# Optimization experiments

Hardware: AMD Instinct MI355X
Metric: run time of the kernel (lower is better)

The kernel has to match this reference:

```python
import jax, jax.numpy as jnp
import numpy as np

N, D, H = 2048, 1024, 16
DH = D // H
LN_EPS = 1e-5


def setup_inputs() -> dict:
    key = jax.random.key(0)
    ks = jax.random.split(key, 12)
    s = 1.0 / np.sqrt(D)
    return {
        "ht": jax.random.normal(ks[0], (N, D), jnp.float32),
        "attention_mask": jnp.ones((1, N), jnp.float32),
        "Wq": jax.random.normal(ks[1], (D, D), jnp.float32) * s,
        "bq": jnp.zeros((D,), jnp.float32),
        "Wk": jax.random.normal(ks[2], (D, D), jnp.float32) * s,
        "bk": jnp.zeros((D,), jnp.float32),
        "Wv": jax.random.normal(ks[3], (D, D), jnp.float32) * s,
        "bv": jnp.zeros((D,), jnp.float32),
        "Wd": jax.random.normal(ks[4], (D, D), jnp.float32) * s,
        "bd": jnp.zeros((D,), jnp.float32),
        "gamma": jnp.ones((D,), jnp.float32),
        "beta": jnp.zeros((D,), jnp.float32),
    }


def reference(ht, attention_mask, Wq, bq, Wk, bk, Wv, bv, Wd, bd, gamma, beta):
    # ht: [N, D] -> batch of 1: [1, N, D]
    x = ht[None]
    # QKV projections, split into heads: [1, N, H, DH]
    q = (x @ Wq.T + bq).reshape(1, N, H, DH)
    k = (x @ Wk.T + bk).reshape(1, N, H, DH)
    v = (x @ Wv.T + bv).reshape(1, N, H, DH)
    # attention scores [1, H, N, N]
    scores = jnp.einsum("bnhd,bmhd->bhnm", q, k) / jnp.sqrt(jnp.asarray(DH, x.dtype))
    # 2D mask -> [B, 1, 1, N], additive form (1 - m) * -10000
    ext_mask = (1.0 - attention_mask)[:, None, None, :] * -10000.0
    scores = scores + ext_mask
    probs = jax.nn.softmax(scores, axis=-1)
    # context [1, N, H, DH] -> [N, D]
    ctx = jnp.einsum("bhnm,bmhd->bnhd", probs, v).reshape(1, N, D)[0]
    # dense + tanh (dropout p=0 is identity) + residual
    sht = jnp.tanh(ctx @ Wd.T + bd) + ht
    # LayerNorm over last dim
    mu = jnp.mean(sht, axis=-1, keepdims=True)
    var = jnp.var(sht, axis=-1, keepdims=True)
    return (sht - mu) / jnp.sqrt(var + LN_EPS) * gamma + beta
```

## Files before the change

kernel.cpp:

```cpp
#include <hip/hip_runtime.h>
#include <hip/hip_bf16.h>
#include <math.h>

#define N_TOK 2048
#define DMODEL 1024
#define NHEAD 16
#define DHEAD 64
#define LN_EPS 1e-5f
#define LOG2E 1.44269504f

typedef __attribute__((ext_vector_type(8))) short short8;
typedef __attribute__((ext_vector_type(4))) short s16x4;
typedef __attribute__((ext_vector_type(4))) float f32x4;
typedef __attribute__((ext_vector_type(16))) float f32x16;

__device__ inline unsigned short f2bf(float f) {
    union { float f; unsigned u; } v; v.f = f;
    unsigned r = v.u + 0x7FFF + ((v.u >> 16) & 1);
    return (unsigned short)(r >> 16);
}

__device__ inline float bf2f(unsigned short b) {
    union { unsigned u; float f; } v; v.u = ((unsigned)b) << 16;
    return v.f;
}

__device__ __forceinline__ unsigned cvtpk_bf16(float lo, float hi) {
    unsigned r;
    asm("v_cvt_pk_bf16_f32 %0, %1, %2" : "=v"(r) : "v"(lo), "v"(hi));
    return r;
}

__device__ __forceinline__ float mx3(float a, float b, float c) {
    return fmaxf(fmaxf(a, b), c);
}

__device__ __forceinline__ void gld16(const unsigned short* g, unsigned short* l) {
    __builtin_amdgcn_global_load_lds(
        (const __attribute__((address_space(1))) unsigned int*)g,
        (__attribute__((address_space(3))) unsigned int*)l, 16, 0, 0);
}

__global__ __launch_bounds__(256) void cvt_all(
    const float* __restrict__ ht, const float* __restrict__ Wq, const float* __restrict__ Wk,
    const float* __restrict__ Wv, const float* __restrict__ Wd, const float* __restrict__ mask,
    unsigned short* __restrict__ Xb, unsigned short* __restrict__ Wqb,
    unsigned short* __restrict__ Wkb, unsigned short* __restrict__ Wvb,
    unsigned short* __restrict__ Wdb, float* __restrict__ madd)
{
    int b = blockIdx.x;
    if (b < 6144) {
        const float* in; unsigned short* out; int off;
        if (b < 2048) { in = ht; out = Xb; off = b * 1024; }
        else {
            int wb = b - 2048; int wi = wb >> 10;
            off = (wb & 1023) * 1024;
            in  = wi == 0 ? Wq  : wi == 1 ? Wk  : wi == 2 ? Wv  : Wd;
            out = wi == 0 ? Wqb : wi == 1 ? Wkb : wi == 2 ? Wvb : Wdb;
        }
        int i = off + threadIdx.x * 4;
        float4 v = *reinterpret_cast<const float4*>(in + i);
        ushort4 o;
        o.x = f2bf(v.x); o.y = f2bf(v.y); o.z = f2bf(v.z); o.w = f2bf(v.w);
        *reinterpret_cast<ushort4*>(out + i) = o;
    } else {
        int i = (b - 6144) * 1024 + threadIdx.x * 4;
        float4 m = *reinterpret_cast<const float4*>(mask + i);
        float4 o;
        o.x = (1.0f - m.x) * (-10000.0f * LOG2E);
        o.y = (1.0f - m.y) * (-10000.0f * LOG2E);
        o.z = (1.0f - m.z) * (-10000.0f * LOG2E);
        o.w = (1.0f - m.w) * (-10000.0f * LOG2E);
        *reinterpret_cast<float4*>(madd + i) = o;
    }
}

__global__ __launch_bounds__(256) void vtrans(const unsigned short* __restrict__ V,
                                              unsigned short* __restrict__ VT) {
    __shared__ unsigned short tile[64][72];
    int n0 = blockIdx.x * 64;
    int d0 = blockIdx.y * 64;
    int t = threadIdx.x;
    int r = t >> 3, c8 = t & 7;
    #pragma unroll
    for (int it = 0; it < 2; ++it) {
        int rr = it * 32 + r;
        short8 v = *reinterpret_cast<const short8*>(V + (size_t)(n0 + rr) * DMODEL + d0 + c8 * 8);
        *reinterpret_cast<short8*>(&tile[rr][c8 * 8]) = v;
    }
    __syncthreads();
    #pragma unroll
    for (int it = 0; it < 2; ++it) {
        int rr = it * 32 + r;
        short8 o;
        #pragma unroll
        for (int j = 0; j < 8; ++j) o[j] = (short)tile[c8 * 8 + j][rr];
        *reinterpret_cast<short8*>(VT + (size_t)(d0 + rr) * N_TOK + n0 + c8 * 8) = o;
    }
}

__global__ __launch_bounds__(256) void gemm_qkv(
    const unsigned short* __restrict__ X,
    const unsigned short* __restrict__ Wq, const unsigned short* __restrict__ Wk,
    const unsigned short* __restrict__ Wv,
    const float* __restrict__ bq, const float* __restrict__ bk, const float* __restrict__ bv,
    unsigned short* __restrict__ Q, unsigned short* __restrict__ K, unsigned short* __restrict__ V)
{
    __shared__ __align__(16) unsigned short As[64 * 64];
    __shared__ __align__(16) unsigned short Bs[128 * 64];
    int row0 = blockIdx.x * 64;
    int col0 = blockIdx.y * 128;
    int mat = col0 >> 10;
    int wcol0 = col0 & 1023;
    const unsigned short* W = mat == 0 ? Wq : (mat == 1 ? Wk : Wv);
    const float* bias = mat == 0 ? bq : (mat == 1 ? bk : bv);
    unsigned short* O = mat == 0 ? Q : (mat == 1 ? K : V);
    float osc = (mat == 0) ? (0.125f * LOG2E) : 1.0f;

    int t = threadIdx.x, w = t >> 6, l = t & 63;
    int lr = l & 15, lk = l >> 4;
    int wc = w * 32;
    int srow = l >> 3, scol = (l & 7) * 8;

    f32x4 acc[4][2] = {};

    for (int k0 = 0; k0 < DMODEL; k0 += 64) {
        #pragma unroll
        for (int c = 0; c < 2; ++c) {
            int ci = (w << 1) | c;
            int r = (ci << 3) | srow;
            gld16(X + (size_t)(row0 + r) * DMODEL + k0 + scol, As + ci * 512);
        }
        #pragma unroll
        for (int c = 0; c < 4; ++c) {
            int ci = (w << 2) | c;
            int r = (ci << 3) | srow;
            gld16(W + (size_t)(wcol0 + r) * DMODEL + k0 + scol, Bs + ci * 512);
        }
        __syncthreads();
        #pragma unroll
        for (int kk = 0; kk < 64; kk += 32) {
            short8 af[4], bf[2];
            #pragma unroll
            for (int m = 0; m < 4; ++m)
                af[m] = *reinterpret_cast<const short8*>(As + (m * 16 + lr) * 64 + kk + (lk << 3));
            #pragma unroll
            for (int n = 0; n < 2; ++n)
                bf[n] = *reinterpret_cast<const short8*>(Bs + (wc + n * 16 + lr) * 64 + kk + (lk << 3));
            #pragma unroll
            for (int m = 0; m < 4; ++m)
                #pragma unroll
                for (int n = 0; n < 2; ++n)
                    acc[m][n] = __builtin_amdgcn_mfma_f32_16x16x32_bf16(af[m], bf[n], acc[m][n], 0, 0, 0);
        }
        __syncthreads();
    }

    #pragma unroll
    for (int n = 0; n < 2; ++n) {
        int ccol = wcol0 + wc + n * 16 + lr;
        float bia = bias[ccol];
        #pragma unroll
        for (int m = 0; m < 4; ++m) {
            #pragma unroll
            for (int r = 0; r < 4; ++r) {
                int rowg = row0 + m * 16 + lk * 4 + r;
                O[(size_t)rowg * DMODEL + ccol] = f2bf((acc[m][n][r] + bia) * osc);
            }
        }
    }
}

__global__ __launch_bounds__(256) void attn32(
    const unsigned short* __restrict__ Q, const unsigned short* __restrict__ K,
    const unsigned short* __restrict__ VT, const float* __restrict__ madd,
    unsigned short* __restrict__ P0, unsigned short* __restrict__ P1,
    float* __restrict__ Mm, float* __restrict__ Ml)
{
    __shared__ __align__(16) unsigned short Kt[2][4096];
    __shared__ __align__(16) unsigned short Vt[2][4096];

    int h = blockIdx.y;
    int hb = h * DHEAD;
    int z = blockIdx.z;
    int kbase = z << 10;
    int t = threadIdx.x, w = t >> 6, l = t & 63;
    int lo5 = l & 31, hi = l >> 5;
    int qw = blockIdx.x * 128 + w * 32;

    short8 qf[4];
    #pragma unroll
    for (int ds = 0; ds < 4; ++ds)
        qf[ds] = *reinterpret_cast<const short8*>(
            Q + (size_t)(qw + lo5) * DMODEL + hb + ds * 16 + hi * 8);

    short8 ones8;
    #pragma unroll
    for (int j = 0; j < 8; ++j) ones8[j] = (short)0x3F80;

    f32x16 ctx0 = {}, ctx1 = {}, ctxS = {};
    float mrow = -1e30f;

#define STAGE(kt_, buf_) do {                                                   \
        int k0s = kbase + (kt_) * 64;                                           \
        _Pragma("unroll")                                                       \
        for (int c = 0; c < 2; ++c) {                                           \
            int ci = (w << 1) | c;                                              \
            int rr = (ci << 3) | (l >> 3);                                      \
            int sc = (((l & 7) ^ (rr & 7)) << 3);                               \
            gld16(K + (size_t)(k0s + rr) * DMODEL + hb + sc, &Kt[buf_][ci * 512]); \
            gld16(VT + (size_t)(hb + rr) * N_TOK + k0s + sc, &Vt[buf_][ci * 512]); \
        }                                                                       \
    } while (0)

    STAGE(0, 0);
    __syncthreads();

    int cb = 0;
    for (int kt = 0; kt < 16; ++kt) {
        f32x16 s0, s1;
        #pragma unroll
        for (int rg = 0; rg < 4; ++rg) {
            f32x4 a = *reinterpret_cast<const f32x4*>(madd + kbase + kt * 64 + 8 * rg + 4 * hi);
            f32x4 b = *reinterpret_cast<const f32x4*>(madd + kbase + kt * 64 + 32 + 8 * rg + 4 * hi);
            #pragma unroll
            for (int j = 0; j < 4; ++j) { s0[4 * rg + j] = a[j]; s1[4 * rg + j] = b[j]; }
        }

        if (kt + 1 < 16) STAGE(kt + 1, cb ^ 1);

        const unsigned short* Kc = &Kt[cb][0];
        const unsigned short* Vc = &Vt[cb][0];

        __builtin_amdgcn_s_setprio(1);
        #pragma unroll
        for (int ds = 0; ds < 4; ++ds) {
            short8 a0 = *reinterpret_cast<const short8*>(
                Kc + (size_t)lo5 * 64 + (((2 * ds + hi) ^ (l & 7)) << 3));
            s0 = __builtin_amdgcn_mfma_f32_32x32x16_bf16(a0, qf[ds], s0, 0, 0, 0);
        }
        #pragma unroll
        for (int ds = 0; ds < 4; ++ds) {
            short8 a1 = *reinterpret_cast<const short8*>(
                Kc + (size_t)(32 + lo5) * 64 + (((2 * ds + hi) ^ (l & 7)) << 3));
            s1 = __builtin_amdgcn_mfma_f32_32x32x16_bf16(a1, qf[ds], s1, 0, 0, 0);
        }
        __builtin_amdgcn_s_setprio(0);

        float u0 = mx3(s0[0], s0[1], s0[2]);
        float u1 = mx3(s0[3], s0[4], s0[5]);
        float u2 = mx3(s0[6], s0[7], s0[8]);
        float u3 = mx3(s0[9], s0[10], s0[11]);
        float u4 = mx3(s0[12], s0[13], s0[14]);
        float u5 = mx3(s0[15], s1[0], s1[1]);
        float u6 = mx3(s1[2], s1[3], s1[4]);
        float u7 = mx3(s1[5], s1[6], s1[7]);
        float u8 = mx3(s1[8], s1[9], s1[10]);
        float u9 = mx3(s1[11], s1[12], s1[13]);
        float ua = fmaxf(s1[14], s1[15]);
        float v0 = mx3(u0, u1, u2);
        float v1 = mx3(u3, u4, u5);
        float v2 = mx3(u6, u7, u8);
        float tm = mx3(v0, v1, mx3(v2, u9, ua));
        tm = fmaxf(tm, __shfl_xor(tm, 32));

        if (__any(tm > mrow + 8.0f)) {
            float mnew = fmaxf(mrow, tm);
            float sc = __builtin_amdgcn_exp2f(mrow - mnew);
            mrow = mnew;
            #pragma unroll
            for (int reg = 0; reg < 16; ++reg) {
                float scr = __shfl(sc, (reg & 3) + 8 * (reg >> 2) + 4 * hi);
                ctx0[reg] *= scr; ctx1[reg] *= scr; ctxS[reg] *= scr;
            }
        }

        unsigned u[2][4][2];
        #pragma unroll
        for (int g = 0; g < 4; ++g) {
            float p0 = __builtin_amdgcn_exp2f(s0[4 * g + 0] - mrow);
            float p1 = __builtin_amdgcn_exp2f(s0[4 * g + 1] - mrow);
            float p2 = __builtin_amdgcn_exp2f(s0[4 * g + 2] - mrow);
            float p3 = __builtin_amdgcn_exp2f(s0[4 * g + 3] - mrow);
            u[0][g][0] = cvtpk_bf16(p0, p1);
            u[0][g][1] = cvtpk_bf16(p2, p3);
            float q0_ = __builtin_amdgcn_exp2f(s1[4 * g + 0] - mrow);
            float q1_ = __builtin_amdgcn_exp2f(s1[4 * g + 1] - mrow);
            float q2_ = __builtin_amdgcn_exp2f(s1[4 * g + 2] - mrow);
            float q3_ = __builtin_amdgcn_exp2f(s1[4 * g + 3] - mrow);
            u[1][g][0] = cvtpk_bf16(q0_, q1_);
            u[1][g][1] = cvtpk_bf16(q2_, q3_);
        }

        short8 pa[4];
        #pragma unroll
        for (int nb = 0; nb < 2; ++nb) {
            #pragma unroll
            for (int ks = 0; ks < 2; ++ks) {
                auto r0 = __builtin_amdgcn_permlane32_swap(u[nb][2 * ks][0], u[nb][2 * ks + 1][0], false, false);
                auto r1 = __builtin_amdgcn_permlane32_swap(u[nb][2 * ks][1], u[nb][2 * ks + 1][1], false, false);
                union { unsigned uu[4]; short8 v; } pu;
                pu.uu[0] = r0[0]; pu.uu[1] = r1[0]; pu.uu[2] = r0[1]; pu.uu[3] = r1[1];
                pa[nb * 2 + ks] = pu.v;
            }
        }

        __builtin_amdgcn_s_setprio(1);
        #pragma unroll
        for (int ks = 0; ks < 4; ++ks) {
            short8 v0 = *reinterpret_cast<const short8*>(
                Vc + (size_t)lo5 * 64 + (((2 * ks + hi) ^ (l & 7)) << 3));
            ctx0 = __builtin_amdgcn_mfma_f32_32x32x16_bf16(pa[ks], v0, ctx0, 0, 0, 0);
            short8 v1 = *reinterpret_cast<const short8*>(
                Vc + (size_t)(32 + lo5) * 64 + (((2 * ks + hi) ^ (l & 7)) << 3));
            ctx1 = __builtin_amdgcn_mfma_f32_32x32x16_bf16(pa[ks], v1, ctx1, 0, 0, 0);
            ctxS = __builtin_amdgcn_mfma_f32_32x32x16_bf16(pa[ks], ones8, ctxS, 0, 0, 0);
        }
        __builtin_amdgcn_s_setprio(0);

        __syncthreads();
        cb ^= 1;
    }
#undef STAGE

    unsigned short* P = z ? P1 : P0;
    #pragma unroll
    for (int reg = 0; reg < 16; ++reg) {
        float inv = 1.0f / ctxS[reg];
        int row = qw + (reg & 3) + 8 * (reg >> 2) + 4 * hi;
        P[(size_t)row * DMODEL + hb + lo5]      = f2bf(ctx0[reg] * inv);
        P[(size_t)row * DMODEL + hb + 32 + lo5] = f2bf(ctx1[reg] * inv);
    }
    int mlb = z * (NHEAD * N_TOK) + h * N_TOK + qw;
    if (l < 32) Mm[mlb + l] = mrow;
    #pragma unroll
    for (int reg = 0; reg < 16; ++reg) {
        int q = (reg & 3) + 8 * (reg >> 2) + 4 * hi;
        if (lo5 == reg) Ml[mlb + q] = ctxS[reg];
    }
}

__global__ __launch_bounds__(256) void attn_combine(
    const unsigned short* __restrict__ P0, const unsigned short* __restrict__ P1,
    const float* __restrict__ Mm, const float* __restrict__ Ml,
    unsigned short* __restrict__ Ctx)
{
    int tok = blockIdx.x;
    int t = threadIdx.x;
    int d = t * 4;
    int h = t >> 4;
    int i0 = h * N_TOK + tok;
    int i1 = NHEAD * N_TOK + i0;
    float m0 = Mm[i0], m1 = Mm[i1];
    float l0 = Ml[i0], l1 = Ml[i1];
    float m = fmaxf(m0, m1);
    float w0 = l0 * __builtin_amdgcn_exp2f(m0 - m);
    float w1 = l1 * __builtin_amdgcn_exp2f(m1 - m);
    float inv = 1.0f / (w0 + w1);
    w0 *= inv; w1 *= inv;
    ushort4 c0 = *reinterpret_cast<const ushort4*>(P0 + (size_t)tok * DMODEL + d);
    ushort4 c1 = *reinterpret_cast<const ushort4*>(P1 + (size_t)tok * DMODEL + d);
    ushort4 o;
    o.x = f2bf(bf2f(c0.x) * w0 + bf2f(c1.x) * w1);
    o.y = f2bf(bf2f(c0.y) * w0 + bf2f(c1.y) * w1);
    o.z = f2bf(bf2f(c0.z) * w0 + bf2f(c1.z) * w1);
    o.w = f2bf(bf2f(c0.w) * w0 + bf2f(c1.w) * w1);
    *reinterpret_cast<ushort4*>(Ctx + (size_t)tok * DMODEL + d) = o;
}

__global__ __launch_bounds__(256) void gemm_dense(
    const unsigned short* __restrict__ X, const unsigned short* __restrict__ W,
    const float* __restrict__ bias, const float* __restrict__ ht,
    float* __restrict__ Sht)
{
    __shared__ __align__(16) unsigned short As[64 * 64];
    __shared__ __align__(16) unsigned short Bs[128 * 64];
    int row0 = blockIdx.x * 64;
    int col0 = blockIdx.y * 128;

    int t = threadIdx.x, w = t >> 6, l = t & 63;
    int lr = l & 15, lk = l >> 4;
    int wc = w * 32;
    int srow = l >> 3, scol = (l & 7) * 8;

    f32x4 acc[4][2] = {};

    for (int k0 = 0; k0 < DMODEL; k0 += 64) {
        #pragma unroll
        for (int c = 0; c < 2; ++c) {
            int ci = (w << 1) | c;
            int r = (ci << 3) | srow;
            gld16(X + (size_t)(row0 + r) * DMODEL + k0 + scol, As + ci * 512);
        }
        #pragma unroll
        for (int c = 0; c < 4; ++c) {
            int ci = (w << 2) | c;
            int r = (ci << 3) | srow;
            gld16(W + (size_t)(col0 + r) * DMODEL + k0 + scol, Bs + ci * 512);
        }
        __syncthreads();
        #pragma unroll
        for (int kk = 0; kk < 64; kk += 32) {
            short8 af[4], bf[2];
            #pragma unroll
            for (int m = 0; m < 4; ++m)
                af[m] = *reinterpret_cast<const short8*>(As + (m * 16 + lr) * 64 + kk + (lk << 3));
            #pragma unroll
            for (int n = 0; n < 2; ++n)
                bf[n] = *reinterpret_cast<const short8*>(Bs + (wc + n * 16 + lr) * 64 + kk + (lk << 3));
            #pragma unroll
            for (int m = 0; m < 4; ++m)
                #pragma unroll
                for (int n = 0; n < 2; ++n)
                    acc[m][n] = __builtin_amdgcn_mfma_f32_16x16x32_bf16(af[m], bf[n], acc[m][n], 0, 0, 0);
        }
        __syncthreads();
    }

    #pragma unroll
    for (int n = 0; n < 2; ++n) {
        int col = col0 + wc + n * 16 + lr;
        float bia = bias[col];
        #pragma unroll
        for (int m = 0; m < 4; ++m) {
            #pragma unroll
            for (int r = 0; r < 4; ++r) {
                int rowg = row0 + m * 16 + lk * 4 + r;
                float x2 = 2.0f * (acc[m][n][r] + bia);
                float th = 1.0f - 2.0f / (1.0f + __expf(x2));
                Sht[(size_t)rowg * DMODEL + col] = th + ht[(size_t)rowg * DMODEL + col];
            }
        }
    }
}

__global__ __launch_bounds__(256) void layernorm(
    const float* __restrict__ S, const float* __restrict__ gamma,
    const float* __restrict__ beta, float* __restrict__ out)
{
    int row = blockIdx.x;
    int t = threadIdx.x;
    const float* x = S + (size_t)row * DMODEL;
    float4 v = *reinterpret_cast<const float4*>(x + t * 4);
    float sum = v.x + v.y + v.z + v.w;
    float sq = v.x * v.x + v.y * v.y + v.z * v.z + v.w * v.w;
    #pragma unroll
    for (int d = 1; d < 64; d <<= 1) { sum += __shfl_xor(sum, d); sq += __shfl_xor(sq, d); }
    __shared__ float ssum[4], ssq[4];
    int w = t >> 6, l = t & 63;
    if (l == 0) { ssum[w] = sum; ssq[w] = sq; }
    __syncthreads();
    sum = ssum[0] + ssum[1] + ssum[2] + ssum[3];
    sq = ssq[0] + ssq[1] + ssq[2] + ssq[3];
    float mu = sum / DMODEL;
    float var = sq / DMODEL - mu * mu;
    float inv = rsqrtf(var + LN_EPS);
    float4 g = *reinterpret_cast<const float4*>(gamma + t * 4);
    float4 b = *reinterpret_cast<const float4*>(beta + t * 4);
    float4 o;
    o.x = (v.x - mu) * inv * g.x + b.x;
    o.y = (v.y - mu) * inv * g.y + b.y;
    o.z = (v.z - mu) * inv * g.z + b.z;
    o.w = (v.w - mu) * inv * g.w + b.w;
    *reinterpret_cast<float4*>(out + (size_t)row * DMODEL + t * 4) = o;
}

extern "C" void kernel_launch(void* const* d_in, const int* in_sizes, int n_in,
                              void* d_out, int out_size, void* d_ws, size_t ws_size,
                              hipStream_t stream) {
    const float* ht   = (const float*)d_in[0];
    const float* mask = (const float*)d_in[1];
    const float* Wq   = (const float*)d_in[2];
    const float* bq   = (const float*)d_in[3];
    const float* Wk   = (const float*)d_in[4];
    const float* bk   = (const float*)d_in[5];
    const float* Wv   = (const float*)d_in[6];
    const float* bv   = (const float*)d_in[7];
    const float* Wd   = (const float*)d_in[8];
    const float* bd   = (const float*)d_in[9];
    const float* gamma= (const float*)d_in[10];
    const float* beta = (const float*)d_in[11];
    float* out = (float*)d_out;

    char* ws = (char*)d_ws;
    const size_t MB = 1024 * 1024;
    unsigned short* Xb  = (unsigned short*)(ws + 0 * MB);
    unsigned short* Wqb = (unsigned short*)(ws + 4 * MB);
    unsigned short* Wkb = (unsigned short*)(ws + 6 * MB);
    unsigned short* Wvb = (unsigned short*)(ws + 8 * MB);
    unsigned short* Wdb = (unsigned short*)(ws + 10 * MB);
    unsigned short* Qb  = (unsigned short*)(ws + 12 * MB);
    unsigned short* Kb  = (unsigned short*)(ws + 16 * MB);
    unsigned short* Vb  = (unsigned short*)(ws + 20 * MB);
    unsigned short* VTb = (unsigned short*)(ws + 24 * MB);
    unsigned short* Ctxb= (unsigned short*)(ws + 28 * MB);
    float* maddb        = (float*)(ws + 32 * MB);
    unsigned short* Pctx0 = Xb;
    unsigned short* Pctx1 = Vb;
    float* Mm           = (float*)(ws + 4 * MB);
    float* Ml           = (float*)(ws + 4 * MB + 256 * 1024);
    float* Sht          = (float*)(ws + 12 * MB);

    cvt_all<<<6146, 256, 0, stream>>>(ht, Wq, Wk, Wv, Wd, mask,
                                      Xb, Wqb, Wkb, Wvb, Wdb, maddb);

    gemm_qkv<<<dim3(32, 24), 256, 0, stream>>>(Xb, Wqb, Wkb, Wvb, bq, bk, bv, Qb, Kb, Vb);

    vtrans<<<dim3(N_TOK / 64, DMODEL / 64), 256, 0, stream>>>(Vb, VTb);

    attn32<<<dim3(N_TOK / 128, NHEAD, 2), 256, 0, stream>>>(
        Qb, Kb, VTb, maddb, Pctx0, Pctx1, Mm, Ml);

    attn_combine<<<N_TOK, 256, 0, stream>>>(Pctx0, Pctx1, Mm, Ml, Ctxb);

    gemm_dense<<<dim3(32, 8), 256, 0, stream>>>(Ctxb, Wdb, bd, ht, Sht);

    layernorm<<<N_TOK, 256, 0, stream>>>(Sht, gamma, beta, out);
}
```

Before: 102.4 us.

## Stage 128-key attention tiles with LDS mask, shrink dense GEMM tile to 64x64

The attention kernel now stages two 64-key subtiles per double-buffer step, halving barrier count, and loads the additive mask into LDS instead of reading it from global memory each iteration. The dense projection GEMM tile shrinks from 64x128 to 64x64, doubling the grid to 512 blocks for better CU occupancy at lower per-block reuse. LDS use in attention roughly doubles, which may reduce occupancy.

```diff
diff --git a/kernel.cpp b/kernel.cpp
--- a/kernel.cpp
+++ b/kernel.cpp
@@ -177,8 +177,9 @@
     unsigned short* __restrict__ P0, unsigned short* __restrict__ P1,
     float* __restrict__ Mm, float* __restrict__ Ml)
 {
-    __shared__ __align__(16) unsigned short Kt[2][4096];
-    __shared__ __align__(16) unsigned short Vt[2][4096];
+    __shared__ __align__(16) unsigned short Kt[2][2][4096];
+    __shared__ __align__(16) unsigned short Vt[2][2][4096];
+    __shared__ __align__(16) float Mt[2][128];
 
     int h = blockIdx.y;
     int hb = h * DHEAD;
@@ -202,121 +203,132 @@
     float mrow = -1e30f;
 
 #define STAGE(kt_, buf_) do {                                                   \
-        int k0s = kbase + (kt_) * 64;                                           \
+        int k0s = kbase + (kt_) * 128;                                          \
         _Pragma("unroll")                                                       \
-        for (int c = 0; c < 2; ++c) {                                           \
-            int ci = (w << 1) | c;                                              \
-            int rr = (ci << 3) | (l >> 3);                                      \
-            int sc = (((l & 7) ^ (rr & 7)) << 3);                               \
-            gld16(K + (size_t)(k0s + rr) * DMODEL + hb + sc, &Kt[buf_][ci * 512]); \
-            gld16(VT + (size_t)(hb + rr) * N_TOK + k0s + sc, &Vt[buf_][ci * 512]); \
+        for (int sub = 0; sub < 2; ++sub) {                                     \
+            _Pragma("unroll")                                                   \
+            for (int c = 0; c < 2; ++c) {                                       \
+                int ci = (w << 1) | c;                                          \
+                int rr = (ci << 3) | (l >> 3);                                  \
+                int sc = (((l & 7) ^ (rr & 7)) << 3);                           \
+                gld16(K + (size_t)(k0s + sub * 64 + rr) * DMODEL + hb + sc,     \
+                      &Kt[buf_][sub][ci * 512]);                                \
+                gld16(VT + (size_t)(hb + rr) * N_TOK + k0s + sub * 64 + sc,     \
+                      &Vt[buf_][sub][ci * 512]);                                \
+            }                                                                   \
         }                                                                       \
+        if (t < 32) gld16((const unsigned short*)(madd + k0s + l * 4),          \
+                          (unsigned short*)&Mt[buf_][0]);                       \
     } while (0)
 
     STAGE(0, 0);
     __syncthreads();
 
     int cb = 0;
-    for (int kt = 0; kt < 16; ++kt) {
-        f32x16 s0, s1;
-        #pragma unroll
-        for (int rg = 0; rg < 4; ++rg) {
-            f32x4 a = *reinterpret_cast<const f32x4*>(madd + kbase + kt * 64 + 8 * rg + 4 * hi);
-            f32x4 b = *reinterpret_cast<const f32x4*>(madd + kbase + kt * 64 + 32 + 8 * rg + 4 * hi);
-            #pragma unroll
-            for (int j = 0; j < 4; ++j) { s0[4 * rg + j] = a[j]; s1[4 * rg + j] = b[j]; }
-        }
-
-        if (kt + 1 < 16) STAGE(kt + 1, cb ^ 1);
-
-        const unsigned short* Kc = &Kt[cb][0];
-        const unsigned short* Vc = &Vt[cb][0];
-
-        __builtin_amdgcn_s_setprio(1);
-        #pragma unroll
-        for (int ds = 0; ds < 4; ++ds) {
-            short8 a0 = *reinterpret_cast<const short8*>(
-                Kc + (size_t)lo5 * 64 + (((2 * ds + hi) ^ (l & 7)) << 3));
-            s0 = __builtin_amdgcn_mfma_f32_32x32x16_bf16(a0, qf[ds], s0, 0, 0, 0);
-        }
-        #pragma unroll
-        for (int ds = 0; ds < 4; ++ds) {
-            short8 a1 = *reinterpret_cast<const short8*>(
-                Kc + (size_t)(32 + lo5) * 64 + (((2 * ds + hi) ^ (l & 7)) << 3));
-            s1 = __builtin_amdgcn_mfma_f32_32x32x16_bf16(a1, qf[ds], s1, 0, 0, 0);
-        }
-        __builtin_amdgcn_s_setprio(0);
-
-        float u0 = mx3(s0[0], s0[1], s0[2]);
-        float u1 = mx3(s0[3], s0[4], s0[5]);
-        float u2 = mx3(s0[6], s0[7], s0[8]);
-        float u3 = mx3(s0[9], s0[10], s0[11]);
-        float u4 = mx3(s0[12], s0[13], s0[14]);
-        float u5 = mx3(s0[15], s1[0], s1[1]);
-        float u6 = mx3(s1[2], s1[3], s1[4]);
-        float u7 = mx3(s1[5], s1[6], s1[7]);
-        float u8 = mx3(s1[8], s1[9], s1[10]);
-        float u9 = mx3(s1[11], s1[12], s1[13]);
-        float ua = fmaxf(s1[14], s1[15]);
-        float v0 = mx3(u0, u1, u2);
-        float v1 = mx3(u3, u4, u5);
-        float v2 = mx3(u6, u7, u8);
-        float tm = mx3(v0, v1, mx3(v2, u9, ua));
-        tm = fmaxf(tm, __shfl_xor(tm, 32));
-
-        if (__any(tm > mrow + 8.0f)) {
-            float mnew = fmaxf(mrow, tm);
-            float sc = __builtin_amdgcn_exp2f(mrow - mnew);
-            mrow = mnew;
-            #pragma unroll
-            for (int reg = 0; reg < 16; ++reg) {
-                float scr = __shfl(sc, (reg & 3) + 8 * (reg >> 2) + 4 * hi);
-                ctx0[reg] *= scr; ctx1[reg] *= scr; ctxS[reg] *= scr;
-            }
-        }
-
-        unsigned u[2][4][2];
-        #pragma unroll
-        for (int g = 0; g < 4; ++g) {
-            float p0 = __builtin_amdgcn_exp2f(s0[4 * g + 0] - mrow);
-            float p1 = __builtin_amdgcn_exp2f(s0[4 * g + 1] - mrow);
-            float p2 = __builtin_amdgcn_exp2f(s0[4 * g + 2] - mrow);
-            float p3 = __builtin_amdgcn_exp2f(s0[4 * g + 3] - mrow);
-            u[0][g][0] = cvtpk_bf16(p0, p1);
-            u[0][g][1] = cvtpk_bf16(p2, p3);
-            float q0_ = __builtin_amdgcn_exp2f(s1[4 * g + 0] - mrow);
-            float q1_ = __builtin_amdgcn_exp2f(s1[4 * g + 1] - mrow);
-            float q2_ = __builtin_amdgcn_exp2f(s1[4 * g + 2] - mrow);
-            float q3_ = __builtin_amdgcn_exp2f(s1[4 * g + 3] - mrow);
-            u[1][g][0] = cvtpk_bf16(q0_, q1_);
-            u[1][g][1] = cvtpk_bf16(q2_, q3_);
-        }
-
-        short8 pa[4];
-        #pragma unroll
-        for (int nb = 0; nb < 2; ++nb) {
-            #pragma unroll
-            for (int ks = 0; ks < 2; ++ks) {
-                auto r0 = __builtin_amdgcn_permlane32_swap(u[nb][2 * ks][0], u[nb][2 * ks + 1][0], false, false);
-                auto r1 = __builtin_amdgcn_permlane32_swap(u[nb][2 * ks][1], u[nb][2 * ks + 1][1], false, false);
-                union { unsigned uu[4]; short8 v; } pu;
-                pu.uu[0] = r0[0]; pu.uu[1] = r1[0]; pu.uu[2] = r0[1]; pu.uu[3] = r1[1];
-                pa[nb * 2 + ks] = pu.v;
-            }
-        }
-
-        __builtin_amdgcn_s_setprio(1);
-        #pragma unroll
-        for (int ks = 0; ks < 4; ++ks) {
-            short8 v0 = *reinterpret_cast<const short8*>(
-                Vc + (size_t)lo5 * 64 + (((2 * ks + hi) ^ (l & 7)) << 3));
-            ctx0 = __builtin_amdgcn_mfma_f32_32x32x16_bf16(pa[ks], v0, ctx0, 0, 0, 0);
-            short8 v1 = *reinterpret_cast<const short8*>(
-                Vc + (size_t)(32 + lo5) * 64 + (((2 * ks + hi) ^ (l & 7)) << 3));
-            ctx1 = __builtin_amdgcn_mfma_f32_32x32x16_bf16(pa[ks], v1, ctx1, 0, 0, 0);
-            ctxS = __builtin_amdgcn_mfma_f32_32x32x16_bf16(pa[ks], ones8, ctxS, 0, 0, 0);
-        }
-        __builtin_amdgcn_s_setprio(0);
+    for (int kt = 0; kt < 8; ++kt) {
+        if (kt + 1 < 8) STAGE(kt + 1, cb ^ 1);
+
+        #pragma unroll
+        for (int sub = 0; sub < 2; ++sub) {
+            const unsigned short* Kc = &Kt[cb][sub][0];
+            const unsigned short* Vc = &Vt[cb][sub][0];
+            const float* Mc = &Mt[cb][sub * 64];
+
+            f32x16 s0, s1;
+            #pragma unroll
+            for (int rg = 0; rg < 4; ++rg) {
+                f32x4 a = *reinterpret_cast<const f32x4*>(Mc + 8 * rg + 4 * hi);
+                f32x4 b = *reinterpret_cast<const f32x4*>(Mc + 32 + 8 * rg + 4 * hi);
+                #pragma unroll
+                for (int j = 0; j < 4; ++j) { s0[4 * rg + j] = a[j]; s1[4 * rg + j] = b[j]; }
+            }
+
+            __builtin_amdgcn_s_setprio(1);
+            #pragma unroll
+            for (int ds = 0; ds < 4; ++ds) {
+                short8 a0 = *reinterpret_cast<const short8*>(
+                    Kc + (size_t)lo5 * 64 + (((2 * ds + hi) ^ (l & 7)) << 3));
+                s0 = __builtin_amdgcn_mfma_f32_32x32x16_bf16(a0, qf[ds], s0, 0, 0, 0);
+            }
+            #pragma unroll
+            for (int ds = 0; ds < 4; ++ds) {
+                short8 a1 = *reinterpret_cast<const short8*>(
+                    Kc + (size_t)(32 + lo5) * 64 + (((2 * ds + hi) ^ (l & 7)) << 3));
+                s1 = __builtin_amdgcn_mfma_f32_32x32x16_bf16(a1, qf[ds], s1, 0, 0, 0);
+            }
+            __builtin_amdgcn_s_setprio(0);
+
+            float u0 = mx3(s0[0], s0[1], s0[2]);
+            float u1 = mx3(s0[3], s0[4], s0[5]);
+            float u2 = mx3(s0[6], s0[7], s0[8]);
+            float u3 = mx3(s0[9], s0[10], s0[11]);
+            float u4 = mx3(s0[12], s0[13], s0[14]);
+            float u5 = mx3(s0[15], s1[0], s1[1]);
+            float u6 = mx3(s1[2], s1[3], s1[4]);
+            float u7 = mx3(s1[5], s1[6], s1[7]);
+            float u8 = mx3(s1[8], s1[9], s1[10]);
+            float u9 = mx3(s1[11], s1[12], s1[13]);
+            float ua = fmaxf(s1[14], s1[15]);
+            float v0_ = mx3(u0, u1, u2);
+            float v1_ = mx3(u3, u4, u5);
+            float v2_ = mx3(u6, u7, u8);
+            float tm = mx3(v0_, v1_, mx3(v2_, u9, ua));
+            tm = fmaxf(tm, __shfl_xor(tm, 32));
+
+            if (__any(tm > mrow + 8.0f)) {
+                float mnew = fmaxf(mrow, tm);
+                float sc = __builtin_amdgcn_exp2f(mrow - mnew);
+                mrow = mnew;
+                #pragma unroll
+                for (int reg = 0; reg < 16; ++reg) {
+                    float scr = __shfl(sc, (reg & 3) + 8 * (reg >> 2) + 4 * hi);
+                    ctx0[reg] *= scr; ctx1[reg] *= scr; ctxS[reg] *= scr;
+                }
+            }
+
+            unsigned u[2][4][2];
+            #pragma unroll
+            for (int g = 0; g < 4; ++g) {
+                float p0 = __builtin_amdgcn_exp2f(s0[4 * g + 0] - mrow);
+                float p1 = __builtin_amdgcn_exp2f(s0[4 * g + 1] - mrow);
+                float p2 = __builtin_amdgcn_exp2f(s0[4 * g + 2] - mrow);
+                float p3 = __builtin_amdgcn_exp2f(s0[4 * g + 3] - mrow);
+                u[0][g][0] = cvtpk_bf16(p0, p1);
+                u[0][g][1] = cvtpk_bf16(p2, p3);
+                float q0_ = __builtin_amdgcn_exp2f(s1[4 * g + 0] - mrow);
+                float q1_ = __builtin_amdgcn_exp2f(s1[4 * g + 1] - mrow);
+                float q2_ = __builtin_amdgcn_exp2f(s1[4 * g + 2] - mrow);
+                float q3_ = __builtin_amdgcn_exp2f(s1[4 * g + 3] - mrow);
+                u[1][g][0] = cvtpk_bf16(q0_, q1_);
+                u[1][g][1] = cvtpk_bf16(q2_, q3_);
+            }
+
+            short8 pa[4];
+            #pragma unroll
+            for (int nb = 0; nb < 2; ++nb) {
+                #pragma unroll
+                for (int ks = 0; ks < 2; ++ks) {
+                    auto r0 = __builtin_amdgcn_permlane32_swap(u[nb][2 * ks][0], u[nb][2 * ks + 1][0], false, false);
+                    auto r1 = __builtin_amdgcn_permlane32_swap(u[nb][2 * ks][1], u[nb][2 * ks + 1][1], false, false);
+                    union { unsigned uu[4]; short8 v; } pu;
+                    pu.uu[0] = r0[0]; pu.uu[1] = r1[0]; pu.uu[2] = r0[1]; pu.uu[3] = r1[1];
+                    pa[nb * 2 + ks] = pu.v;
+                }
+            }
+
+            __builtin_amdgcn_s_setprio(1);
+            #pragma unroll
+            for (int ks = 0; ks < 4; ++ks) {
+                short8 v0 = *reinterpret_cast<const short8*>(
+                    Vc + (size_t)lo5 * 64 + (((2 * ks + hi) ^ (l & 7)) << 3));
+                ctx0 = __builtin_amdgcn_mfma_f32_32x32x16_bf16(pa[ks], v0, ctx0, 0, 0, 0);
+                short8 v1 = *reinterpret_cast<const short8*>(
+                    Vc + (size_t)(32 + lo5) * 64 + (((2 * ks + hi) ^ (l & 7)) << 3));
+                ctx1 = __builtin_amdgcn_mfma_f32_32x32x16_bf16(pa[ks], v1, ctx1, 0, 0, 0);
+                ctxS = __builtin_amdgcn_mfma_f32_32x32x16_bf16(pa[ks], ones8, ctxS, 0, 0, 0);
+            }
+            __builtin_amdgcn_s_setprio(0);
+        }
 
         __syncthreads();
         cb ^= 1;
@@ -374,16 +386,16 @@
     float* __restrict__ Sht)
 {
     __shared__ __align__(16) unsigned short As[64 * 64];
-    __shared__ __align__(16) unsigned short Bs[128 * 64];
+    __shared__ __align__(16) unsigned short Bs[64 * 64];
     int row0 = blockIdx.x * 64;
-    int col0 = blockIdx.y * 128;
+    int col0 = blockIdx.y * 64;
 
     int t = threadIdx.x, w = t >> 6, l = t & 63;
     int lr = l & 15, lk = l >> 4;
-    int wc = w * 32;
+    int wc = w * 16;
     int srow = l >> 3, scol = (l & 7) * 8;
 
-    f32x4 acc[4][2] = {};
+    f32x4 acc[4] = {};
 
     for (int k0 = 0; k0 < DMODEL; k0 += 64) {
         #pragma unroll
@@ -391,45 +403,33 @@
             int ci = (w << 1) | c;
             int r = (ci << 3) | srow;
             gld16(X + (size_t)(row0 + r) * DMODEL + k0 + scol, As + ci * 512);
-        }
-        #pragma unroll
-        for (int c = 0; c < 4; ++c) {
-            int ci = (w << 2) | c;
-            int r = (ci << 3) | srow;
             gld16(W + (size_t)(col0 + r) * DMODEL + k0 + scol, Bs + ci * 512);
         }
         __syncthreads();
         #pragma unroll
         for (int kk = 0; kk < 64; kk += 32) {
-            short8 af[4], bf[2];
+            short8 af[4], bf0;
             #pragma unroll
             for (int m = 0; m < 4; ++m)
                 af[m] = *reinterpret_cast<const short8*>(As + (m * 16 + lr) * 64 + kk + (lk << 3));
-            #pragma unroll
-            for (int n = 0; n < 2; ++n)
-                bf[n] = *reinterpret_cast<const short8*>(Bs + (wc + n * 16 + lr) * 64 + kk + (lk << 3));
+            bf0 = *reinterpret_cast<const short8*>(Bs + (wc + lr) * 64 + kk + (lk << 3));
             #pragma unroll
             for (int m = 0; m < 4; ++m)
-                #pragma unroll
-                for (int n = 0; n < 2; ++n)
-                    acc[m][n] = __builtin_amdgcn_mfma_f32_16x16x32_bf16(af[m], bf[n], acc[m][n], 0, 0, 0);
+                acc[m] = __builtin_amdgcn_mfma_f32_16x16x32_bf16(af[m], bf0, acc[m], 0, 0, 0);
         }
         __syncthreads();
     }
 
-    #pragma unroll
-    for (int n = 0; n < 2; ++n) {
-        int col = col0 + wc + n * 16 + lr;
-        float bia = bias[col];
-        #pragma unroll
-        for (int m = 0; m < 4; ++m) {
-            #pragma unroll
-            for (int r = 0; r < 4; ++r) {
-                int rowg = row0 + m * 16 + lk * 4 + r;
-                float x2 = 2.0f * (acc[m][n][r] + bia);
-                float th = 1.0f - 2.0f / (1.0f + __expf(x2));
-                Sht[(size_t)rowg * DMODEL + col] = th + ht[(size_t)rowg * DMODEL + col];
-            }
+    int col = col0 + wc + lr;
+    float bia = bias[col];
+    #pragma unroll
+    for (int m = 0; m < 4; ++m) {
+        #pragma unroll
+        for (int r = 0; r < 4; ++r) {
+            int rowg = row0 + m * 16 + lk * 4 + r;
+            float x2 = 2.0f * (acc[m][r] + bia);
+            float th = 1.0f - 2.0f / (1.0f + __expf(x2));
+            Sht[(size_t)rowg * DMODEL + col] = th + ht[(size_t)rowg * DMODEL + col];
         }
     }
 }
@@ -513,7 +513,7 @@
 
     attn_combine<<<N_TOK, 256, 0, stream>>>(Pctx0, Pctx1, Mm, Ml, Ctxb);
 
-    gemm_dense<<<dim3(32, 8), 256, 0, stream>>>(Ctxb, Wdb, bd, ht, Sht);
+    gemm_dense<<<dim3(32, 16), 256, 0, stream>>>(Ctxb, Wdb, bd, ht, Sht);
 
     layernorm<<<N_TOK, 256, 0, stream>>>(Sht, gamma, beta, out);
 }
```

New measurement: 97.36 us. 4.9% less time.
